# Performance work log

Measured on AMD Instinct MI355X. Metric: run time of the kernel, lower is better.

## Reference

```python
import jax, jax.numpy as jnp
import numpy as np

D_E = 128
D_R = 128  # must equal D_E for the original torch code to typecheck
BN_EPS = 1e-5


def setup_inputs() -> dict:
    key = jax.random.key(0)
    ks = jax.random.split(key, 8)
    B, S = 16, 2048
    h = jax.random.normal(ks[0], (B, S, D_E), dtype=jnp.float32)
    r = jax.random.normal(ks[1], (B, S, D_R), dtype=jnp.float32)
    t = jax.random.normal(ks[2], (B, S, D_E), dtype=jnp.float32)
    # Xavier-uniform core tensor W: (d_r, d_e, d_e)
    limit = float(np.sqrt(6.0 / (D_R + D_E * D_E)))
    W = jax.random.uniform(ks[3], (D_R, D_E, D_E), minval=-limit, maxval=limit, dtype=jnp.float32)
    # BatchNorm1d params/buffers (inference mode)
    gamma0 = jnp.ones((D_E,), jnp.float32)
    beta0 = jnp.zeros((D_E,), jnp.float32)
    mean0 = 0.1 * jax.random.normal(ks[4], (D_E,), dtype=jnp.float32)
    var0 = jnp.abs(1.0 + 0.1 * jax.random.normal(ks[5], (D_E,), dtype=jnp.float32))
    gamma1 = jnp.ones((D_E,), jnp.float32)
    beta1 = jnp.zeros((D_E,), jnp.float32)
    mean1 = 0.1 * jax.random.normal(ks[6], (D_E,), dtype=jnp.float32)
    var1 = jnp.abs(1.0 + 0.1 * jax.random.normal(ks[7], (D_E,), dtype=jnp.float32))
    return {"h": h, "r": r, "t": t, "W": W,
            "gamma0": gamma0, "beta0": beta0, "mean0": mean0, "var0": var0,
            "gamma1": gamma1, "beta1": beta1, "mean1": mean1, "var1": var1}


def reference(h, r, t, W, gamma0, beta0, mean0, var0, gamma1, beta1, mean1, var1):
    B, S, D = h.shape  # D == d_e == d_r
    N = B * S
    # BatchNorm1d in eval mode over last dim; dropout is identity in eval.
    h_bn = (h - mean0) * jax.lax.rsqrt(var0 + BN_EPS) * gamma0 + beta0
    t_bn = (t - mean1) * jax.lax.rsqrt(var1 + BN_EPS) * gamma1 + beta1
    r2 = r.reshape(N, D)
    # torch.matmul((N,d_r), (d_r,d_e,d_e)) broadcasts -> shape (d_r, N, d_e):
    #   out[k, n, j] = sum_i r2[n, i] * W[k, i, j]
    # followed by .view(N, d_e, d_e) which reinterprets the flat buffer.
    W_mat = jnp.einsum('ni,kij->knj', r2, W).reshape(N, D, D)  # (N, d_e, d_e) after scrambled view
    # hr[n, j] = sum_d h_bn[n, d] * W_mat[n, d, j]
    hr = jnp.einsum('nd,ndj->nj', h_bn.reshape(N, D), W_mat)
    scores = jnp.sum(hr * t_bn.reshape(N, D), axis=-1)  # (N,)
    return scores.reshape(B, S)
```

## Files before the change

### kernel.cpp

```cpp
#include <hip/hip_runtime.h>


typedef __attribute__((ext_vector_type(8))) short bf16x8;
typedef __attribute__((ext_vector_type(4))) short s16x4;
typedef __attribute__((ext_vector_type(4))) float f32x4;

#define DPAD 136
#define BN_EPS 1e-5f

__device__ inline unsigned short f2bf(float f) {
  unsigned u = __builtin_bit_cast(unsigned, f);
  u += 0x7FFFu + ((u >> 16) & 1u);
  return (unsigned short)(u >> 16);
}
__device__ inline float bf2f(unsigned short h) {
  unsigned u = ((unsigned)h) << 16;
  return __builtin_bit_cast(float, u);
}
__device__ inline unsigned pack2bf(float lo, float hi) {
  return (unsigned)f2bf(lo) | ((unsigned)f2bf(hi) << 16);
}

__global__ __launch_bounds__(256) void k_stageA(
    const float* __restrict__ t, const float* __restrict__ W,
    const float* __restrict__ gamma1, const float* __restrict__ beta1,
    const float* __restrict__ mean1, const float* __restrict__ var1,
    unsigned short* __restrict__ V) {
  __shared__ short LA[128 * DPAD];
  __shared__ short LB[128 * DPAD];
  const int tid = threadIdx.x;
  const int c = tid & 31;
  const int rr = tid >> 5;
  const int wv_ = tid >> 6;
  const int lane = tid & 63;
  const int l16 = lane & 15;
  const int quad = lane >> 4;

  const int k = blockIdx.x >> 1;
  const int half = blockIdx.x & 1;
  const int rowbase = k * 256 + half * 128;

  f32x4 g  = *(const f32x4*)(gamma1 + c * 4);
  f32x4 be = *(const f32x4*)(beta1  + c * 4);
  f32x4 mu = *(const f32x4*)(mean1  + c * 4);
  f32x4 va = *(const f32x4*)(var1   + c * 4);
  f32x4 sc, bi;
  for (int q = 0; q < 4; ++q) {
    sc[q] = g[q] * rsqrtf(va[q] + BN_EPS);
    bi[q] = be[q] - mu[q] * sc[q];
  }
  const float* tbase = t + (size_t)rowbase * 128;
  const float* wbase = W + (size_t)k * 16384;
  for (int it = 0; it < 16; ++it) {
    const int m = it * 8 + rr;
    f32x4 tv = *(const f32x4*)(tbase + m * 128 + c * 4);
    s16x4 tb;
    for (int q = 0; q < 4; ++q) tb[q] = (short)f2bf(tv[q] * sc[q] + bi[q]);
    *(s16x4*)(&LA[m * DPAD + c * 4]) = tb;
    f32x4 wvv = *(const f32x4*)(wbase + m * 128 + c * 4);
    s16x4 wb;
    for (int q = 0; q < 4; ++q) wb[q] = (short)f2bf(wvv[q]);
    *(s16x4*)(&LB[m * DPAD + c * 4]) = wb;
  }
  __syncthreads();

  f32x4 acc[2][8];
  for (int mt = 0; mt < 2; ++mt)
    for (int nt = 0; nt < 8; ++nt) acc[mt][nt] = (f32x4){0.f, 0.f, 0.f, 0.f};

  for (int ks = 0; ks < 4; ++ks) {
    const int K0 = ks * 32 + quad * 8;
    bf16x8 a[2], b[8];
    for (int mt = 0; mt < 2; ++mt)
      a[mt] = *(const bf16x8*)(&LA[(wv_ * 32 + mt * 16 + l16) * DPAD + K0]);
    for (int nt = 0; nt < 8; ++nt)
      b[nt] = *(const bf16x8*)(&LB[(nt * 16 + l16) * DPAD + K0]);
    for (int mt = 0; mt < 2; ++mt)
      for (int nt = 0; nt < 8; ++nt)
        acc[mt][nt] = __builtin_amdgcn_mfma_f32_16x16x32_bf16(b[nt], a[mt], acc[mt][nt], 0, 0, 0);
  }

  for (int mt = 0; mt < 2; ++mt) {
    const size_t np = (size_t)(rowbase + wv_ * 32 + mt * 16 + l16) * 128;
    for (int nt = 0; nt < 8; ++nt) {
      unsigned two[2];
      two[0] = pack2bf(acc[mt][nt][0], acc[mt][nt][1]);
      two[1] = pack2bf(acc[mt][nt][2], acc[mt][nt][3]);
      *(uint2*)(V + np + nt * 16 + quad * 4) = *(uint2*)two;
    }
  }
}

__global__ __launch_bounds__(256) void k_bdot(
    const float* __restrict__ h, const float* __restrict__ r,
    const float* __restrict__ gamma0, const float* __restrict__ beta0,
    const float* __restrict__ mean0, const float* __restrict__ var0,
    const unsigned short* __restrict__ V, float* __restrict__ out) {
  __shared__ short LA[128 * DPAD];
  __shared__ short LB[128 * DPAD];
  const int tid = threadIdx.x;
  const int c = tid & 31;
  const int rr = tid >> 5;
  const int wv_ = tid >> 6;
  const int lane = tid & 63;
  const int l16 = lane & 15;
  const int quad = lane >> 4;

  const int low = blockIdx.x;

  f32x4 g  = *(const f32x4*)(gamma0 + c * 4);
  f32x4 be = *(const f32x4*)(beta0  + c * 4);
  f32x4 mu = *(const f32x4*)(mean0  + c * 4);
  f32x4 va = *(const f32x4*)(var0   + c * 4);
  f32x4 sc, bi;
  for (int q = 0; q < 4; ++q) {
    sc[q] = g[q] * rsqrtf(va[q] + BN_EPS);
    bi[q] = be[q] - mu[q] * sc[q];
  }
  for (int it = 0; it < 16; ++it) {
    const int kk = it * 8 + rr;
    f32x4 hv = *(const f32x4*)(h + ((size_t)(kk * 256 + low)) * 128 + c * 4);
    s16x4 hb;
    for (int q = 0; q < 4; ++q) hb[q] = (short)f2bf(hv[q] * sc[q] + bi[q]);
    *(s16x4*)(&LA[kk * DPAD + c * 4]) = hb;
  }
  for (int it = 0; it < 4; ++it) {
    const int a0 = it * 32 + rr * 4;
    f32x4 rv[4];
    for (int v = 0; v < 4; ++v)
      rv[v] = *(const f32x4*)(r + ((size_t)(low * 128 + a0 + v)) * 128 + c * 4);
    for (int u = 0; u < 4; ++u) {
      s16x4 w;
      for (int v = 0; v < 4; ++v) w[v] = (short)f2bf(rv[v][u]);
      *(s16x4*)(&LB[(c * 4 + u) * DPAD + a0]) = w;
    }
  }
  __syncthreads();

  f32x4 acc[2][8];
  for (int mt = 0; mt < 2; ++mt)
    for (int nt = 0; nt < 8; ++nt) acc[mt][nt] = (f32x4){0.f, 0.f, 0.f, 0.f};

  for (int ks = 0; ks < 4; ++ks) {
    const int K0 = ks * 32 + quad * 8;
    bf16x8 a[2], b[8];
    for (int mt = 0; mt < 2; ++mt)
      a[mt] = *(const bf16x8*)(&LA[(wv_ * 32 + mt * 16 + l16) * DPAD + K0]);
    for (int nt = 0; nt < 8; ++nt)
      b[nt] = *(const bf16x8*)(&LB[(nt * 16 + l16) * DPAD + K0]);
    for (int mt = 0; mt < 2; ++mt)
      for (int nt = 0; nt < 8; ++nt)
        acc[mt][nt] = __builtin_amdgcn_mfma_f32_16x16x32_bf16(b[nt], a[mt], acc[mt][nt], 0, 0, 0);
  }

  for (int mt = 0; mt < 2; ++mt) {
    const int kk = wv_ * 32 + mt * 16 + l16;
    const size_t np = ((size_t)kk * 256 + low) * 128;
    float s = 0.f;
    for (int nt = 0; nt < 8; ++nt) {
      const uint2 vv = *(const uint2*)(V + np + nt * 16 + quad * 4);
      s += acc[mt][nt][0] * bf2f((unsigned short)(vv.x & 0xFFFFu));
      s += acc[mt][nt][1] * bf2f((unsigned short)(vv.x >> 16));
      s += acc[mt][nt][2] * bf2f((unsigned short)(vv.y & 0xFFFFu));
      s += acc[mt][nt][3] * bf2f((unsigned short)(vv.y >> 16));
    }
    s += __shfl_xor(s, 16, 64);
    s += __shfl_xor(s, 32, 64);
    if (quad == 0) out[(size_t)kk * 256 + low] = s;
  }
}

extern "C" void kernel_launch(void* const* d_in, const int* in_sizes, int n_in,
                              void* d_out, int out_size, void* d_ws, size_t ws_size,
                              hipStream_t stream) {
  const float* h      = (const float*)d_in[0];
  const float* r      = (const float*)d_in[1];
  const float* t      = (const float*)d_in[2];
  const float* W      = (const float*)d_in[3];
  const float* gamma0 = (const float*)d_in[4];
  const float* beta0  = (const float*)d_in[5];
  const float* mean0  = (const float*)d_in[6];
  const float* var0   = (const float*)d_in[7];
  const float* gamma1 = (const float*)d_in[8];
  const float* beta1  = (const float*)d_in[9];
  const float* mean1  = (const float*)d_in[10];
  const float* var1   = (const float*)d_in[11];
  float* out = (float*)d_out;

  unsigned short* V = (unsigned short*)d_ws;

  k_stageA<<<256, 256, 0, stream>>>(t, W, gamma1, beta1, mean1, var1, V);
  k_bdot<<<256, 256, 0, stream>>>(h, r, gamma0, beta0, mean0, var0, V, out);
}
```

Baseline: 115.9 us.

## Split both kernels into half-size M tiles with 512 blocks and XCD-aware mapping

Each kernel now processes 64 rows per block instead of 128, which doubles the grid to 512 workgroups so the GPU's CUs get better coverage. LDS per block shrinks, and launch_bounds(256,2) asks for two blocks per CU. An XCD-aware block remap groups neighbouring tiles onto the same XCD for L2 reuse, and s_setprio raises wave priority around the MFMA loop. The cost is that W (in stageA) and r (in bdot) are now reloaded and converted by twice as many blocks.

```diff
diff --git a/kernel.cpp b/kernel.cpp
--- a/kernel.cpp
+++ b/kernel.cpp
@@ -21,12 +21,14 @@
   return (unsigned)f2bf(lo) | ((unsigned)f2bf(hi) << 16);
 }
 
-__global__ __launch_bounds__(256) void k_stageA(
+__device__ inline int xcd_map(int bid) { return (bid & 7) * 64 + (bid >> 3); }
+
+__global__ __launch_bounds__(256, 2) void k_stageA(
     const float* __restrict__ t, const float* __restrict__ W,
     const float* __restrict__ gamma1, const float* __restrict__ beta1,
     const float* __restrict__ mean1, const float* __restrict__ var1,
     unsigned short* __restrict__ V) {
-  __shared__ short LA[128 * DPAD];
+  __shared__ short LA[64 * DPAD];
   __shared__ short LB[128 * DPAD];
   const int tid = threadIdx.x;
   const int c = tid & 31;
@@ -36,9 +38,10 @@
   const int l16 = lane & 15;
   const int quad = lane >> 4;
 
-  const int k = blockIdx.x >> 1;
-  const int half = blockIdx.x & 1;
-  const int rowbase = k * 256 + half * 128;
+  const int wg = xcd_map(blockIdx.x);
+  const int k = wg >> 2;
+  const int quarter = wg & 3;
+  const int rowbase = k * 256 + quarter * 64;
 
   f32x4 g  = *(const f32x4*)(gamma1 + c * 4);
   f32x4 be = *(const f32x4*)(beta1  + c * 4);
@@ -51,12 +54,17 @@
   }
   const float* tbase = t + (size_t)rowbase * 128;
   const float* wbase = W + (size_t)k * 16384;
-  for (int it = 0; it < 16; ++it) {
+#pragma unroll
+  for (int it = 0; it < 8; ++it) {
     const int m = it * 8 + rr;
     f32x4 tv = *(const f32x4*)(tbase + m * 128 + c * 4);
     s16x4 tb;
     for (int q = 0; q < 4; ++q) tb[q] = (short)f2bf(tv[q] * sc[q] + bi[q]);
     *(s16x4*)(&LA[m * DPAD + c * 4]) = tb;
+  }
+#pragma unroll
+  for (int it = 0; it < 16; ++it) {
+    const int m = it * 8 + rr;
     f32x4 wvv = *(const f32x4*)(wbase + m * 128 + c * 4);
     s16x4 wb;
     for (int q = 0; q < 4; ++q) wb[q] = (short)f2bf(wvv[q]);
@@ -64,39 +72,41 @@
   }
   __syncthreads();
 
-  f32x4 acc[2][8];
-  for (int mt = 0; mt < 2; ++mt)
-    for (int nt = 0; nt < 8; ++nt) acc[mt][nt] = (f32x4){0.f, 0.f, 0.f, 0.f};
-
+  f32x4 acc[8];
+#pragma unroll
+  for (int nt = 0; nt < 8; ++nt) acc[nt] = (f32x4){0.f, 0.f, 0.f, 0.f};
+
+  __builtin_amdgcn_s_setprio(1);
+#pragma unroll
   for (int ks = 0; ks < 4; ++ks) {
     const int K0 = ks * 32 + quad * 8;
-    bf16x8 a[2], b[8];
-    for (int mt = 0; mt < 2; ++mt)
-      a[mt] = *(const bf16x8*)(&LA[(wv_ * 32 + mt * 16 + l16) * DPAD + K0]);
+    bf16x8 a = *(const bf16x8*)(&LA[(wv_ * 16 + l16) * DPAD + K0]);
+    bf16x8 b[8];
+#pragma unroll
     for (int nt = 0; nt < 8; ++nt)
       b[nt] = *(const bf16x8*)(&LB[(nt * 16 + l16) * DPAD + K0]);
-    for (int mt = 0; mt < 2; ++mt)
-      for (int nt = 0; nt < 8; ++nt)
-        acc[mt][nt] = __builtin_amdgcn_mfma_f32_16x16x32_bf16(b[nt], a[mt], acc[mt][nt], 0, 0, 0);
-  }
-
-  for (int mt = 0; mt < 2; ++mt) {
-    const size_t np = (size_t)(rowbase + wv_ * 32 + mt * 16 + l16) * 128;
-    for (int nt = 0; nt < 8; ++nt) {
-      unsigned two[2];
-      two[0] = pack2bf(acc[mt][nt][0], acc[mt][nt][1]);
-      two[1] = pack2bf(acc[mt][nt][2], acc[mt][nt][3]);
-      *(uint2*)(V + np + nt * 16 + quad * 4) = *(uint2*)two;
-    }
-  }
-}
-
-__global__ __launch_bounds__(256) void k_bdot(
+#pragma unroll
+    for (int nt = 0; nt < 8; ++nt)
+      acc[nt] = __builtin_amdgcn_mfma_f32_16x16x32_bf16(b[nt], a, acc[nt], 0, 0, 0);
+  }
+  __builtin_amdgcn_s_setprio(0);
+
+  const size_t np = (size_t)(rowbase + wv_ * 16 + l16) * 128;
+#pragma unroll
+  for (int nt = 0; nt < 8; ++nt) {
+    unsigned two[2];
+    two[0] = pack2bf(acc[nt][0], acc[nt][1]);
+    two[1] = pack2bf(acc[nt][2], acc[nt][3]);
+    *(uint2*)(V + np + nt * 16 + quad * 4) = *(uint2*)two;
+  }
+}
+
+__global__ __launch_bounds__(256, 2) void k_bdot(
     const float* __restrict__ h, const float* __restrict__ r,
     const float* __restrict__ gamma0, const float* __restrict__ beta0,
     const float* __restrict__ mean0, const float* __restrict__ var0,
     const unsigned short* __restrict__ V, float* __restrict__ out) {
-  __shared__ short LA[128 * DPAD];
+  __shared__ short LA[64 * DPAD];
   __shared__ short LB[128 * DPAD];
   const int tid = threadIdx.x;
   const int c = tid & 31;
@@ -106,7 +116,10 @@
   const int l16 = lane & 15;
   const int quad = lane >> 4;
 
-  const int low = blockIdx.x;
+  const int wg = xcd_map(blockIdx.x);
+  const int low = wg >> 1;
+  const int half = wg & 1;
+  const int kkbase = half * 64;
 
   f32x4 g  = *(const f32x4*)(gamma0 + c * 4);
   f32x4 be = *(const f32x4*)(beta0  + c * 4);
@@ -117,13 +130,15 @@
     sc[q] = g[q] * rsqrtf(va[q] + BN_EPS);
     bi[q] = be[q] - mu[q] * sc[q];
   }
-  for (int it = 0; it < 16; ++it) {
-    const int kk = it * 8 + rr;
-    f32x4 hv = *(const f32x4*)(h + ((size_t)(kk * 256 + low)) * 128 + c * 4);
+#pragma unroll
+  for (int it = 0; it < 8; ++it) {
+    const int kkloc = it * 8 + rr;
+    f32x4 hv = *(const f32x4*)(h + ((size_t)(kkbase + kkloc) * 256 + low) * 128 + c * 4);
     s16x4 hb;
     for (int q = 0; q < 4; ++q) hb[q] = (short)f2bf(hv[q] * sc[q] + bi[q]);
-    *(s16x4*)(&LA[kk * DPAD + c * 4]) = hb;
-  }
+    *(s16x4*)(&LA[kkloc * DPAD + c * 4]) = hb;
+  }
+#pragma unroll
   for (int it = 0; it < 4; ++it) {
     const int a0 = it * 32 + rr * 4;
     f32x4 rv[4];
@@ -137,37 +152,39 @@
   }
   __syncthreads();
 
-  f32x4 acc[2][8];
-  for (int mt = 0; mt < 2; ++mt)
-    for (int nt = 0; nt < 8; ++nt) acc[mt][nt] = (f32x4){0.f, 0.f, 0.f, 0.f};
-
+  f32x4 acc[8];
+#pragma unroll
+  for (int nt = 0; nt < 8; ++nt) acc[nt] = (f32x4){0.f, 0.f, 0.f, 0.f};
+
+  __builtin_amdgcn_s_setprio(1);
+#pragma unroll
   for (int ks = 0; ks < 4; ++ks) {
     const int K0 = ks * 32 + quad * 8;
-    bf16x8 a[2], b[8];
-    for (int mt = 0; mt < 2; ++mt)
-      a[mt] = *(const bf16x8*)(&LA[(wv_ * 32 + mt * 16 + l16) * DPAD + K0]);
+    bf16x8 a = *(const bf16x8*)(&LA[(wv_ * 16 + l16) * DPAD + K0]);
+    bf16x8 b[8];
+#pragma unroll
     for (int nt = 0; nt < 8; ++nt)
       b[nt] = *(const bf16x8*)(&LB[(nt * 16 + l16) * DPAD + K0]);
-    for (int mt = 0; mt < 2; ++mt)
-      for (int nt = 0; nt < 8; ++nt)
-        acc[mt][nt] = __builtin_amdgcn_mfma_f32_16x16x32_bf16(b[nt], a[mt], acc[mt][nt], 0, 0, 0);
-  }
-
-  for (int mt = 0; mt < 2; ++mt) {
-    const int kk = wv_ * 32 + mt * 16 + l16;
-    const size_t np = ((size_t)kk * 256 + low) * 128;
-    float s = 0.f;
-    for (int nt = 0; nt < 8; ++nt) {
-      const uint2 vv = *(const uint2*)(V + np + nt * 16 + quad * 4);
-      s += acc[mt][nt][0] * bf2f((unsigned short)(vv.x & 0xFFFFu));
-      s += acc[mt][nt][1] * bf2f((unsigned short)(vv.x >> 16));
-      s += acc[mt][nt][2] * bf2f((unsigned short)(vv.y & 0xFFFFu));
-      s += acc[mt][nt][3] * bf2f((unsigned short)(vv.y >> 16));
-    }
-    s += __shfl_xor(s, 16, 64);
-    s += __shfl_xor(s, 32, 64);
-    if (quad == 0) out[(size_t)kk * 256 + low] = s;
-  }
+#pragma unroll
+    for (int nt = 0; nt < 8; ++nt)
+      acc[nt] = __builtin_amdgcn_mfma_f32_16x16x32_bf16(b[nt], a, acc[nt], 0, 0, 0);
+  }
+  __builtin_amdgcn_s_setprio(0);
+
+  const int kk = kkbase + wv_ * 16 + l16;
+  const size_t np = ((size_t)kk * 256 + low) * 128;
+  float s = 0.f;
+#pragma unroll
+  for (int nt = 0; nt < 8; ++nt) {
+    const uint2 vv = *(const uint2*)(V + np + nt * 16 + quad * 4);
+    s += acc[nt][0] * bf2f((unsigned short)(vv.x & 0xFFFFu));
+    s += acc[nt][1] * bf2f((unsigned short)(vv.x >> 16));
+    s += acc[nt][2] * bf2f((unsigned short)(vv.y & 0xFFFFu));
+    s += acc[nt][3] * bf2f((unsigned short)(vv.y >> 16));
+  }
+  s += __shfl_xor(s, 16, 64);
+  s += __shfl_xor(s, 32, 64);
+  if (quad == 0) out[(size_t)kk * 256 + low] = s;
 }
 
 extern "C" void kernel_launch(void* const* d_in, const int* in_sizes, int n_in,
@@ -189,6 +206,6 @@
 
   unsigned short* V = (unsigned short*)d_ws;
 
-  k_stageA<<<256, 256, 0, stream>>>(t, W, gamma1, beta1, mean1, var1, V);
-  k_bdot<<<256, 256, 0, stream>>>(h, r, gamma0, beta0, mean0, var0, V, out);
-}
+  k_stageA<<<512, 256, 0, stream>>>(t, W, gamma1, beta1, mean1, var1, V);
+  k_bdot<<<512, 256, 0, stream>>>(h, r, gamma0, beta0, mean0, var0, V, out);
+}
```

Result: no change. 117.0 us (+1.0%).
